# Kernel optimization log

Measured on AMD Instinct MI355X. Metric: run time of the kernel, lower is better.

The kernel has to match this reference:

```python
import jax, jax.numpy as jnp
import numpy as np

# Hyperparameters (match init_kwargs)
COORD_DIM = 3
GRID_MIN = -1.0
GRID_MAX = 1.0
N_LEVELS = 16
N_FEATS = 2
LOG2_T = 19
TABLE_SIZE = 2 ** LOG2_T
BASE_RES = 16
FINEST_RES = 512
BSZ = 1048576

_growth = np.exp((np.log(FINEST_RES) - np.log(BASE_RES)) / (N_LEVELS - 1))
RESOLUTIONS = [int(np.floor(BASE_RES * _growth ** i)) for i in range(N_LEVELS)]

# InstantNGP spatial-hash primes (uint32: low bits of the product/xor are
# identical to the int64 computation, and we only keep LOG2_T low bits).
PRIMES = jnp.asarray(np.array([1, 2654435761, 805459861], dtype=np.uint32))
# (8, 3) binary corner offsets of a unit cube.
OFFSETS = jnp.asarray(
    np.array([[(k >> d) & 1 for d in range(COORD_DIM)] for k in range(2 ** COORD_DIM)],
             dtype=np.uint32))
MASK = jnp.uint32(TABLE_SIZE - 1)


def _embed_level(x, table, resolution):
    """x: (B, 3) coords; table: (T, F) hash table. Returns (B, F)."""
    grid_size = (GRID_MAX - GRID_MIN) / resolution
    rel = (x - GRID_MIN) / grid_size                       # (B, 3)
    idx0 = jnp.clip(jnp.floor(rel), 0, resolution - 1)     # bottom-left vertex index
    w = rel - idx0                                         # (B, 3) interp weights in [0,1]
    vidx = idx0.astype(jnp.uint32)[:, None, :] + OFFSETS[None]   # (B, 8, 3)
    # spatial hash: xor of (index * prime) over dims, masked to table size
    vp = vidx * PRIMES[None, None, :]
    h = (vp[..., 0] ^ vp[..., 1] ^ vp[..., 2]) & MASK      # (B, 8) uint32
    verts = table[h.astype(jnp.int32)]                      # (B, 8, F) gather
    # d-linear interpolation weights per corner
    wts = jnp.prod(jnp.where(OFFSETS[None] == 1, w[:, None, :], 1.0 - w[:, None, :]),
                   axis=-1)                                 # (B, 8)
    return jnp.einsum('bv,bvf->bf', wts, verts)             # (B, F)


def setup_inputs() -> dict:
    k1, k2 = jax.random.split(jax.random.key(0))
    x = jax.random.uniform(k1, (BSZ, COORD_DIM), jnp.float32,
                           minval=GRID_MIN, maxval=GRID_MAX)
    embeddings = jax.random.uniform(k2, (N_LEVELS, TABLE_SIZE, N_FEATS), jnp.float32,
                                    minval=-1e-4, maxval=1e-4)
    return {"x": x, "embeddings": embeddings}


def reference(x, embeddings):
    outs = [_embed_level(x, embeddings[i], RESOLUTIONS[i]) for i in range(N_LEVELS)]
    return jnp.concatenate(outs, axis=-1)  # (B, L*F)
```

## Files before the change

kernel.cpp:

```cpp
#include <hip/hip_runtime.h>
#include <hip/hip_fp16.h>
#include <stdint.h>


#define N_LEVELS   16
#define LOG2_T     19
#define TABLE_SIZE (1u << LOG2_T)
#define HASH_MASK  (TABLE_SIZE - 1u)
#define P1 2654435761u
#define P2 805459861u
#define N_DENSE    8

__constant__ int   c_res[N_LEVELS]   = {16, 20, 25, 32, 40, 50, 64, 80,
                                        101, 128, 161, 203, 256, 322, 406, 512};
__constant__ float c_scale[N_LEVELS] = {8.0f, 10.0f, 12.5f, 16.0f, 20.0f, 25.0f,
                                        32.0f, 40.0f, 50.5f, 64.0f, 80.5f, 101.5f,
                                        128.0f, 161.0f, 203.0f, 256.0f};
__constant__ uint32_t c_dim[N_DENSE]  = {17, 21, 26, 33, 41, 51, 65, 81};
__constant__ uint32_t c_doff[N_DENSE] = {0, 4913, 14174, 31750,
                                         67687, 136608, 269259, 543884};
#define DENSE_TOTAL 1075325u

__global__ __launch_bounds__(256) void conv_hash(
    const float2* __restrict__ emb, uint32_t* __restrict__ ht, int total)
{
    int i = blockIdx.x * 256 + threadIdx.x;
    if (i >= total) return;
    float2 v = emb[(size_t)N_DENSE * TABLE_SIZE + i];
    __half2 h = __float22half2_rn(v);
    ht[i] = *(uint32_t*)&h;
}

__global__ __launch_bounds__(256) void conv_dense(
    const float2* __restrict__ emb, uint32_t* __restrict__ dn)
{
    int l = blockIdx.y;
    uint32_t v = blockIdx.x * 256 + threadIdx.x;
    uint32_t S = c_dim[l];
    if (v >= S * S * S) return;
    uint32_t ix = v % S;
    uint32_t r  = v / S;
    uint32_t iy = r % S;
    uint32_t iz = r / S;
    uint32_t h  = (ix ^ (iy * P1) ^ (iz * P2)) & HASH_MASK;
    float2 val  = emb[(size_t)l * TABLE_SIZE + h];
    __half2 hv  = __float22half2_rn(val);
    dn[c_doff[l] + v] = *(uint32_t*)&hv;
}

__device__ __forceinline__ void do_point(
    int l, int b, int npts,
    const float* __restrict__ x,
    const uint32_t* __restrict__ ht,
    const uint32_t* __restrict__ dn,
    uint32_t* __restrict__ tmp)
{
    if (b >= npts) return;
    size_t xb = (size_t)b * 3;
    float xx = x[xb], xy = x[xb + 1], xz = x[xb + 2];

    float scale = c_scale[l];
    float hi    = (float)c_res[l] - 1.0f;

    float rx = (xx + 1.0f) * scale;
    float ry = (xy + 1.0f) * scale;
    float rz = (xz + 1.0f) * scale;

    float fx = fminf(fmaxf(floorf(rx), 0.0f), hi);
    float fy = fminf(fmaxf(floorf(ry), 0.0f), hi);
    float fz = fminf(fmaxf(floorf(rz), 0.0f), hi);

    float wx = rx - fx, wy = ry - fy, wz = rz - fz;
    uint32_t ix = (uint32_t)fx, iy = (uint32_t)fy, iz = (uint32_t)fz;

    uint32_t u0, u1, u2, u3, u4, u5, u6, u7;
    if (l < N_DENSE) {
        uint32_t S    = c_dim[l];
        uint32_t base = c_doff[l] + (iz * S + iy) * S + ix;
        uint32_t S2   = S * S;
        u0 = dn[base];           u1 = dn[base + 1];
        u2 = dn[base + S];       u3 = dn[base + S + 1];
        u4 = dn[base + S2];      u5 = dn[base + S2 + 1];
        u6 = dn[base + S2 + S];  u7 = dn[base + S2 + S + 1];
    } else {
        const uint32_t* __restrict__ tb = ht + (size_t)(l - N_DENSE) * TABLE_SIZE;
        uint32_t a0 = ix,      a1 = ix + 1u;
        uint32_t b0 = iy * P1, b1 = b0 + P1;
        uint32_t c0 = iz * P2, c1 = c0 + P2;
        u0 = tb[(a0 ^ b0 ^ c0) & HASH_MASK];
        u1 = tb[(a1 ^ b0 ^ c0) & HASH_MASK];
        u2 = tb[(a0 ^ b1 ^ c0) & HASH_MASK];
        u3 = tb[(a1 ^ b1 ^ c0) & HASH_MASK];
        u4 = tb[(a0 ^ b0 ^ c1) & HASH_MASK];
        u5 = tb[(a1 ^ b0 ^ c1) & HASH_MASK];
        u6 = tb[(a0 ^ b1 ^ c1) & HASH_MASK];
        u7 = tb[(a1 ^ b1 ^ c1) & HASH_MASK];
    }

    float2 v0 = __half22float2(*(__half2*)&u0);
    float2 v1 = __half22float2(*(__half2*)&u1);
    float2 v2 = __half22float2(*(__half2*)&u2);
    float2 v3 = __half22float2(*(__half2*)&u3);
    float2 v4 = __half22float2(*(__half2*)&u4);
    float2 v5 = __half22float2(*(__half2*)&u5);
    float2 v6 = __half22float2(*(__half2*)&u6);
    float2 v7 = __half22float2(*(__half2*)&u7);

    float ux = 1.0f - wx, uy = 1.0f - wy, uz = 1.0f - wz;
    float w0 = ux * uy * uz, w1 = wx * uy * uz;
    float w2 = ux * wy * uz, w3 = wx * wy * uz;
    float w4 = ux * uy * wz, w5 = wx * uy * wz;
    float w6 = ux * wy * wz, w7 = wx * wy * wz;

    float o0 = w0 * v0.x + w1 * v1.x + w2 * v2.x + w3 * v3.x
             + w4 * v4.x + w5 * v5.x + w6 * v6.x + w7 * v7.x;
    float o1 = w0 * v0.y + w1 * v1.y + w2 * v2.y + w3 * v3.y
             + w4 * v4.y + w5 * v5.y + w6 * v6.y + w7 * v7.y;

    __half2 r = __float22half2_rn(make_float2(o0, o1));
    tmp[(size_t)l * npts + b] = *(uint32_t*)&r;
}

__global__ __launch_bounds__(256) void gather_lvl(
    const float* __restrict__ x,
    const uint32_t* __restrict__ ht,
    const uint32_t* __restrict__ dn,
    uint32_t* __restrict__ tmp, int npts)
{
    const int l  = blockIdx.y;
    const int bA = blockIdx.x * 512 + threadIdx.x;
    do_point(l, bA,       npts, x, ht, dn, tmp);
    do_point(l, bA + 256, npts, x, ht, dn, tmp);
}

__global__ __launch_bounds__(256) void transpose_k(
    const uint32_t* __restrict__ tmp, float4* __restrict__ out4, int npts)
{
    __shared__ uint32_t sm[N_LEVELS][514];

    const int b0 = blockIdx.x * 512;
    const int t  = threadIdx.x;

    if (b0 + 512 <= npts) {
        #pragma unroll
        for (int l = 0; l < N_LEVELS; ++l) {
            uint2 u = *(const uint2*)&tmp[(size_t)l * npts + b0 + 2 * t];
            sm[l][2 * t]     = u.x;
            sm[l][2 * t + 1] = u.y;
        }
        __syncthreads();
        #pragma unroll
        for (int k = 0; k < 16; ++k) {
            int q = k * 256 + t;
            int p = q >> 3;
            int j = q & 7;
            uint32_t a = sm[2 * j][p], b = sm[2 * j + 1][p];
            float2 f0 = __half22float2(*(__half2*)&a);
            float2 f1 = __half22float2(*(__half2*)&b);
            out4[(size_t)(b0 + p) * 8 + j] = make_float4(f0.x, f0.y, f1.x, f1.y);
        }
    } else {
        for (int l = 0; l < N_LEVELS; ++l) {
            for (int s = 0; s < 2; ++s) {
                int b = b0 + 2 * t + s;
                if (b < npts) sm[l][2 * t + s] = tmp[(size_t)l * npts + b];
            }
        }
        __syncthreads();
        for (int k = 0; k < 16; ++k) {
            int q = k * 256 + t;
            int p = q >> 3, j = q & 7;
            if (b0 + p < npts) {
                uint32_t a = sm[2 * j][p], b = sm[2 * j + 1][p];
                float2 f0 = __half22float2(*(__half2*)&a);
                float2 f1 = __half22float2(*(__half2*)&b);
                out4[(size_t)(b0 + p) * 8 + j] = make_float4(f0.x, f0.y, f1.x, f1.y);
            }
        }
    }
}

__global__ __launch_bounds__(256) void hash_embed_direct(
    const float* __restrict__ x, const float* __restrict__ emb,
    float2* __restrict__ out, int npts)
{
    int t = blockIdx.x * 256 + threadIdx.x;
    int l = t & 15, b = t >> 4;
    if (b >= npts) return;
    size_t xb = (size_t)b * 3;
    float scale = c_scale[l], hi = (float)c_res[l] - 1.0f;
    float rx = (x[xb] + 1.0f) * scale, ry = (x[xb+1] + 1.0f) * scale, rz = (x[xb+2] + 1.0f) * scale;
    float fx = fminf(fmaxf(floorf(rx), 0.0f), hi);
    float fy = fminf(fmaxf(floorf(ry), 0.0f), hi);
    float fz = fminf(fmaxf(floorf(rz), 0.0f), hi);
    float wx = rx - fx, wy = ry - fy, wz = rz - fz;
    uint32_t ix = (uint32_t)fx, iy = (uint32_t)fy, iz = (uint32_t)fz;
    uint32_t a0 = ix, a1 = ix + 1u, b0 = iy * P1, b1 = b0 + P1, c0 = iz * P2, c1 = c0 + P2;
    const float2* tb = (const float2*)emb + (size_t)l * TABLE_SIZE;
    float2 v0 = tb[(a0^b0^c0)&HASH_MASK], v1 = tb[(a1^b0^c0)&HASH_MASK];
    float2 v2 = tb[(a0^b1^c0)&HASH_MASK], v3 = tb[(a1^b1^c0)&HASH_MASK];
    float2 v4 = tb[(a0^b0^c1)&HASH_MASK], v5 = tb[(a1^b0^c1)&HASH_MASK];
    float2 v6 = tb[(a0^b1^c1)&HASH_MASK], v7 = tb[(a1^b1^c1)&HASH_MASK];
    float ux = 1.0f - wx, uy = 1.0f - wy, uz = 1.0f - wz;
    float w0 = ux*uy*uz, w1 = wx*uy*uz, w2 = ux*wy*uz, w3 = wx*wy*uz;
    float w4 = ux*uy*wz, w5 = wx*uy*wz, w6 = ux*wy*wz, w7 = wx*wy*wz;
    float o0 = w0*v0.x+w1*v1.x+w2*v2.x+w3*v3.x+w4*v4.x+w5*v5.x+w6*v6.x+w7*v7.x;
    float o1 = w0*v0.y+w1*v1.y+w2*v2.y+w3*v3.y+w4*v4.y+w5*v5.y+w6*v6.y+w7*v7.y;
    out[(size_t)b * N_LEVELS + l] = make_float2(o0, o1);
}

extern "C" void kernel_launch(void* const* d_in, const int* in_sizes, int n_in,
                              void* d_out, int out_size, void* d_ws, size_t ws_size,
                              hipStream_t stream)
{
    const float*  x   = (const float*)d_in[0];
    const float2* emb = (const float2*)d_in[1];
    int npts = in_sizes[0] / 3;

    size_t tmp_bytes = (size_t)npts * N_LEVELS * 4;
    size_t ht_bytes  = (size_t)N_DENSE * TABLE_SIZE * 4;
    size_t dn_bytes  = (size_t)DENSE_TOTAL * 4;
    size_t need      = tmp_bytes + ht_bytes + dn_bytes;

    if (ws_size >= need) {
        uint32_t* tmp = (uint32_t*)d_ws;
        uint32_t* ht  = (uint32_t*)((char*)d_ws + tmp_bytes);
        uint32_t* dn  = (uint32_t*)((char*)d_ws + tmp_bytes + ht_bytes);

        int ht_total = N_DENSE * TABLE_SIZE;
        hipLaunchKernelGGL(conv_hash, dim3((ht_total + 255) / 256), dim3(256),
                           0, stream, emb, ht, ht_total);
        hipLaunchKernelGGL(conv_dense, dim3(2077, N_DENSE), dim3(256),
                           0, stream, emb, dn);
        hipLaunchKernelGGL(gather_lvl, dim3((npts + 511) / 512, N_LEVELS), dim3(256),
                           0, stream, (const float*)x, ht, dn, tmp, npts);
        hipLaunchKernelGGL(transpose_k, dim3((npts + 511) / 512), dim3(256),
                           0, stream, tmp, (float4*)d_out, npts);
    } else {
        int total = npts * N_LEVELS;
        hipLaunchKernelGGL(hash_embed_direct, dim3((total + 255) / 256), dim3(256),
                           0, stream, (const float*)x, (const float*)emb,
                           (float2*)d_out, npts);
    }
}
```

Baseline: 491.0 us.

## Precompute per-cell 8-corner fp16 blocks for dense levels

New measurement: 460.1 us. -6.3%, faster.

```diff
diff --git a/kernel.cpp b/kernel.cpp
--- a/kernel.cpp
+++ b/kernel.cpp
@@ -16,10 +16,15 @@
 __constant__ float c_scale[N_LEVELS] = {8.0f, 10.0f, 12.5f, 16.0f, 20.0f, 25.0f,
                                         32.0f, 40.0f, 50.5f, 64.0f, 80.5f, 101.5f,
                                         128.0f, 161.0f, 203.0f, 256.0f};
+
 __constant__ uint32_t c_dim[N_DENSE]  = {17, 21, 26, 33, 41, 51, 65, 81};
 __constant__ uint32_t c_doff[N_DENSE] = {0, 4913, 14174, 31750,
                                          67687, 136608, 269259, 543884};
 #define DENSE_TOTAL 1075325u
+
+__constant__ uint32_t c_coff[N_DENSE] = {0, 4096, 12096, 27721,
+                                         60489, 124489, 249489, 511633};
+#define CELL_TOTAL 1023633u
 
 __global__ __launch_bounds__(256) void conv_hash(
     const float2* __restrict__ emb, uint32_t* __restrict__ ht, int total)
@@ -29,6 +34,44 @@
     float2 v = emb[(size_t)N_DENSE * TABLE_SIZE + i];
     __half2 h = __float22half2_rn(v);
     ht[i] = *(uint32_t*)&h;
+}
+
+__global__ __launch_bounds__(256) void conv_cell(
+    const float2* __restrict__ emb, uint4* __restrict__ cg)
+{
+    int l = blockIdx.y;
+    uint32_t c = blockIdx.x * 256 + threadIdx.x;
+    uint32_t R = (uint32_t)c_res[l];
+    if (c >= R * R * R) return;
+    uint32_t ix = c % R;
+    uint32_t r  = c / R;
+    uint32_t iy = r % R;
+    uint32_t iz = r / R;
+
+    const float2* __restrict__ tb = emb + (size_t)l * TABLE_SIZE;
+    uint32_t a0 = ix,      a1 = ix + 1u;
+    uint32_t b0 = iy * P1, b1 = b0 + P1;
+    uint32_t d0 = iz * P2, d1 = d0 + P2;
+
+    float2 f0 = tb[(a0 ^ b0 ^ d0) & HASH_MASK];
+    float2 f1 = tb[(a1 ^ b0 ^ d0) & HASH_MASK];
+    float2 f2 = tb[(a0 ^ b1 ^ d0) & HASH_MASK];
+    float2 f3 = tb[(a1 ^ b1 ^ d0) & HASH_MASK];
+    float2 f4 = tb[(a0 ^ b0 ^ d1) & HASH_MASK];
+    float2 f5 = tb[(a1 ^ b0 ^ d1) & HASH_MASK];
+    float2 f6 = tb[(a0 ^ b1 ^ d1) & HASH_MASK];
+    float2 f7 = tb[(a1 ^ b1 ^ d1) & HASH_MASK];
+
+    __half2 h0 = __float22half2_rn(f0), h1 = __float22half2_rn(f1);
+    __half2 h2 = __float22half2_rn(f2), h3 = __float22half2_rn(f3);
+    __half2 h4 = __float22half2_rn(f4), h5 = __float22half2_rn(f5);
+    __half2 h6 = __float22half2_rn(f6), h7 = __float22half2_rn(f7);
+
+    uint32_t base = 2u * (c_coff[l] + c);
+    cg[base]      = make_uint4(*(uint32_t*)&h0, *(uint32_t*)&h1,
+                               *(uint32_t*)&h2, *(uint32_t*)&h3);
+    cg[base + 1u] = make_uint4(*(uint32_t*)&h4, *(uint32_t*)&h5,
+                               *(uint32_t*)&h6, *(uint32_t*)&h7);
 }
 
 __global__ __launch_bounds__(256) void conv_dense(
@@ -48,11 +91,13 @@
     dn[c_doff[l] + v] = *(uint32_t*)&hv;
 }
 
+template <bool CELL>
 __device__ __forceinline__ void do_point(
     int l, int b, int npts,
     const float* __restrict__ x,
     const uint32_t* __restrict__ ht,
     const uint32_t* __restrict__ dn,
+    const uint4*    __restrict__ cg,
     uint32_t* __restrict__ tmp)
 {
     if (b >= npts) return;
@@ -60,28 +105,38 @@
     float xx = x[xb], xy = x[xb + 1], xz = x[xb + 2];
 
     float scale = c_scale[l];
-    float hi    = (float)c_res[l] - 1.0f;
+    float hiv   = (float)c_res[l] - 1.0f;
 
     float rx = (xx + 1.0f) * scale;
     float ry = (xy + 1.0f) * scale;
     float rz = (xz + 1.0f) * scale;
 
-    float fx = fminf(fmaxf(floorf(rx), 0.0f), hi);
-    float fy = fminf(fmaxf(floorf(ry), 0.0f), hi);
-    float fz = fminf(fmaxf(floorf(rz), 0.0f), hi);
+    float fx = fminf(fmaxf(floorf(rx), 0.0f), hiv);
+    float fy = fminf(fmaxf(floorf(ry), 0.0f), hiv);
+    float fz = fminf(fmaxf(floorf(rz), 0.0f), hiv);
 
     float wx = rx - fx, wy = ry - fy, wz = rz - fz;
     uint32_t ix = (uint32_t)fx, iy = (uint32_t)fy, iz = (uint32_t)fz;
 
     uint32_t u0, u1, u2, u3, u4, u5, u6, u7;
     if (l < N_DENSE) {
-        uint32_t S    = c_dim[l];
-        uint32_t base = c_doff[l] + (iz * S + iy) * S + ix;
-        uint32_t S2   = S * S;
-        u0 = dn[base];           u1 = dn[base + 1];
-        u2 = dn[base + S];       u3 = dn[base + S + 1];
-        u4 = dn[base + S2];      u5 = dn[base + S2 + 1];
-        u6 = dn[base + S2 + S];  u7 = dn[base + S2 + S + 1];
+        if constexpr (CELL) {
+            uint32_t R    = (uint32_t)c_res[l];
+            uint32_t cidx = (iz * R + iy) * R + ix;
+            uint32_t base = 2u * (c_coff[l] + cidx);
+            uint4 lo = cg[base];
+            uint4 hi = cg[base + 1u];
+            u0 = lo.x; u1 = lo.y; u2 = lo.z; u3 = lo.w;
+            u4 = hi.x; u5 = hi.y; u6 = hi.z; u7 = hi.w;
+        } else {
+            uint32_t S    = c_dim[l];
+            uint32_t base = c_doff[l] + (iz * S + iy) * S + ix;
+            uint32_t S2   = S * S;
+            u0 = dn[base];           u1 = dn[base + 1];
+            u2 = dn[base + S];       u3 = dn[base + S + 1];
+            u4 = dn[base + S2];      u5 = dn[base + S2 + 1];
+            u6 = dn[base + S2 + S];  u7 = dn[base + S2 + S + 1];
+        }
     } else {
         const uint32_t* __restrict__ tb = ht + (size_t)(l - N_DENSE) * TABLE_SIZE;
         uint32_t a0 = ix,      a1 = ix + 1u;
@@ -121,16 +176,18 @@
     tmp[(size_t)l * npts + b] = *(uint32_t*)&r;
 }
 
+template <bool CELL>
 __global__ __launch_bounds__(256) void gather_lvl(
     const float* __restrict__ x,
     const uint32_t* __restrict__ ht,
     const uint32_t* __restrict__ dn,
+    const uint4*    __restrict__ cg,
     uint32_t* __restrict__ tmp, int npts)
 {
     const int l  = blockIdx.y;
     const int bA = blockIdx.x * 512 + threadIdx.x;
-    do_point(l, bA,       npts, x, ht, dn, tmp);
-    do_point(l, bA + 256, npts, x, ht, dn, tmp);
+    do_point<CELL>(l, bA,       npts, x, ht, dn, cg, tmp);
+    do_point<CELL>(l, bA + 256, npts, x, ht, dn, cg, tmp);
 }
 
 __global__ __launch_bounds__(256) void transpose_k(
@@ -145,8 +202,7 @@
         #pragma unroll
         for (int l = 0; l < N_LEVELS; ++l) {
             uint2 u = *(const uint2*)&tmp[(size_t)l * npts + b0 + 2 * t];
-            sm[l][2 * t]     = u.x;
-            sm[l][2 * t + 1] = u.y;
+            *(uint2*)&sm[l][2 * t] = u;
         }
         __syncthreads();
         #pragma unroll
@@ -188,11 +244,11 @@
     int l = t & 15, b = t >> 4;
     if (b >= npts) return;
     size_t xb = (size_t)b * 3;
-    float scale = c_scale[l], hi = (float)c_res[l] - 1.0f;
+    float scale = c_scale[l], hiv = (float)c_res[l] - 1.0f;
     float rx = (x[xb] + 1.0f) * scale, ry = (x[xb+1] + 1.0f) * scale, rz = (x[xb+2] + 1.0f) * scale;
-    float fx = fminf(fmaxf(floorf(rx), 0.0f), hi);
-    float fy = fminf(fmaxf(floorf(ry), 0.0f), hi);
-    float fz = fminf(fmaxf(floorf(rz), 0.0f), hi);
+    float fx = fminf(fmaxf(floorf(rx), 0.0f), hiv);
+    float fy = fminf(fmaxf(floorf(ry), 0.0f), hiv);
+    float fz = fminf(fmaxf(floorf(rz), 0.0f), hiv);
     float wx = rx - fx, wy = ry - fy, wz = rz - fz;
     uint32_t ix = (uint32_t)fx, iy = (uint32_t)fy, iz = (uint32_t)fz;
     uint32_t a0 = ix, a1 = ix + 1u, b0 = iy * P1, b1 = b0 + P1, c0 = iz * P2, c1 = c0 + P2;
@@ -219,21 +275,37 @@
 
     size_t tmp_bytes = (size_t)npts * N_LEVELS * 4;
     size_t ht_bytes  = (size_t)N_DENSE * TABLE_SIZE * 4;
+    size_t cg_bytes  = (size_t)CELL_TOTAL * 32;
     size_t dn_bytes  = (size_t)DENSE_TOTAL * 4;
-    size_t need      = tmp_bytes + ht_bytes + dn_bytes;
-
-    if (ws_size >= need) {
+
+    int ht_total = N_DENSE * TABLE_SIZE;
+
+    if (ws_size >= tmp_bytes + ht_bytes + cg_bytes) {
+        uint32_t* tmp = (uint32_t*)d_ws;
+        uint32_t* ht  = (uint32_t*)((char*)d_ws + tmp_bytes);
+        uint4*    cg  = (uint4*)   ((char*)d_ws + tmp_bytes + ht_bytes);
+
+        hipLaunchKernelGGL(conv_hash, dim3((ht_total + 255) / 256), dim3(256),
+                           0, stream, emb, ht, ht_total);
+        hipLaunchKernelGGL(conv_cell, dim3(2000, N_DENSE), dim3(256),
+                           0, stream, emb, cg);
+        hipLaunchKernelGGL(HIP_KERNEL_NAME(gather_lvl<true>),
+                           dim3((npts + 511) / 512, N_LEVELS), dim3(256),
+                           0, stream, x, ht, (const uint32_t*)nullptr, cg, tmp, npts);
+        hipLaunchKernelGGL(transpose_k, dim3((npts + 511) / 512), dim3(256),
+                           0, stream, tmp, (float4*)d_out, npts);
+    } else if (ws_size >= tmp_bytes + ht_bytes + dn_bytes) {
         uint32_t* tmp = (uint32_t*)d_ws;
         uint32_t* ht  = (uint32_t*)((char*)d_ws + tmp_bytes);
         uint32_t* dn  = (uint32_t*)((char*)d_ws + tmp_bytes + ht_bytes);
 
-        int ht_total = N_DENSE * TABLE_SIZE;
         hipLaunchKernelGGL(conv_hash, dim3((ht_total + 255) / 256), dim3(256),
                            0, stream, emb, ht, ht_total);
         hipLaunchKernelGGL(conv_dense, dim3(2077, N_DENSE), dim3(256),
                            0, stream, emb, dn);
-        hipLaunchKernelGGL(gather_lvl, dim3((npts + 511) / 512, N_LEVELS), dim3(256),
-                           0, stream, (const float*)x, ht, dn, tmp, npts);
+        hipLaunchKernelGGL(HIP_KERNEL_NAME(gather_lvl<false>),
+                           dim3((npts + 511) / 512, N_LEVELS), dim3(256),
+                           0, stream, x, ht, dn, (const uint4*)nullptr, tmp, npts);
         hipLaunchKernelGGL(transpose_k, dim3((npts + 511) / 512), dim3(256),
                            0, stream, tmp, (float4*)d_out, npts);
     } else {
```
